# Performance work log

Measured on AMD Instinct MI355X. Metric: run time of the kernel, lower is better.

Reference implementation:

```python
import jax, jax.numpy as jnp
import numpy as np

N, E, IN, HID, OUT = 50000, 800000, 128, 256, 128
NMASK = 25000  # int(0.5 * N)
EPS = 1e-5


def setup_inputs() -> dict:
    key = jax.random.key(0)
    ks = jax.random.split(key, 8)

    def glorot(k, shape):
        lim = float(np.sqrt(6.0 / (shape[0] + shape[1])))
        return jax.random.uniform(k, shape, jnp.float32, -lim, lim)

    x = jax.random.normal(ks[0], (N, IN), jnp.float32)
    edge_index = jax.random.randint(ks[1], (2, E), 0, N, dtype=jnp.int32)
    mask_nodes = jax.random.permutation(ks[2], N)[:NMASK].astype(jnp.int32)
    return {
        "x": x,
        "edge_index": edge_index,
        "mask_nodes": mask_nodes,
        "mask_token": jnp.zeros((IN,), jnp.float32),
        "W1": glorot(ks[3], (IN, HID)), "b1": jnp.zeros((HID,), jnp.float32),
        "g1": jnp.ones((HID,), jnp.float32), "be1": jnp.zeros((HID,), jnp.float32),
        "a1": jnp.full((1,), 0.25, jnp.float32),
        "W2": glorot(ks[4], (HID, OUT)), "b2": jnp.zeros((OUT,), jnp.float32),
        "g2": jnp.ones((OUT,), jnp.float32), "be2": jnp.zeros((OUT,), jnp.float32),
        "a2": jnp.full((1,), 0.25, jnp.float32),
        "Wd": glorot(ks[5], (OUT, IN)), "bd": jnp.zeros((IN,), jnp.float32),
        "gd": jnp.ones((IN,), jnp.float32), "bed": jnp.zeros((IN,), jnp.float32),
        "ad": jnp.full((1,), 0.25, jnp.float32),
    }


def _gcn_conv(h, W, b, src, dst, dinv):
    # PyG GCNConv with self-loops: out = D^-1/2 (A+I) D^-1/2 (h W) + b
    h = h @ W
    coef = dinv[src] * dinv[dst]                      # [E]
    agg = jnp.zeros_like(h).at[dst].add(h[src] * coef[:, None])
    agg = agg + h * (dinv * dinv)[:, None]            # self-loop term
    return agg + b


def _bn_prelu(h, g, be, a):
    # BatchNorm (training-mode batch stats, biased var) + PReLU
    mu = jnp.mean(h, axis=0)
    var = jnp.mean((h - mu) ** 2, axis=0)
    h = (h - mu) * jax.lax.rsqrt(var + EPS) * g + be
    return jnp.where(h >= 0, h, a * h)


def reference(x, edge_index, mask_nodes, mask_token,
              W1, b1, g1, be1, a1,
              W2, b2, g2, be2, a2,
              Wd, bd, gd, bed, ad):
    src, dst = edge_index[0], edge_index[1]
    # degree with self-loops (shared by all conv layers on the same graph)
    deg = jnp.zeros((N,), x.dtype).at[dst].add(1.0) + 1.0
    dinv = jax.lax.rsqrt(deg)

    target = jax.lax.stop_gradient(x[mask_nodes])      # detached recon target

    # mask: x[mask] = 0 then += token  ->  set to token
    h = x.at[mask_nodes].set(mask_token)

    # online encoder: 2 layers of GCNConv -> BN -> PReLU
    h = _bn_prelu(_gcn_conv(h, W1, b1, src, dst, dinv), g1, be1, a1)
    h = _bn_prelu(_gcn_conv(h, W2, b2, src, dst, dinv), g2, be2, a2)

    # re-mask encoded representation
    h = h.at[mask_nodes].set(0.0)

    # decoder: 1 layer
    re_x = _bn_prelu(_gcn_conv(h, Wd, bd, src, dst, dinv), gd, bed, ad)

    # sce loss (alpha=1) on masked nodes
    p = re_x[mask_nodes]
    p = p / jnp.maximum(jnp.linalg.norm(p, axis=-1, keepdims=True), 1e-12)
    t = target / jnp.maximum(jnp.linalg.norm(target, axis=-1, keepdims=True), 1e-12)
    loss = jnp.mean(1.0 - jnp.sum(p * t, axis=-1))
    return loss
```

## Files before the change

### kernel.cpp

```cpp
#include <hip/hip_runtime.h>
#include <hip/hip_bf16.h>
#include <math.h>


#define EPSV 1e-5f
#define CAP2 16
#define DCAP 64

typedef __attribute__((ext_vector_type(8))) short short8v;
typedef __attribute__((ext_vector_type(4))) float f32x4;
typedef __attribute__((ext_vector_type(2))) float f32x2;

static __device__ __forceinline__ void atomAddF(float* p, float v) {
  unsafeAtomicAdd(p, v);
}

static __device__ __forceinline__ unsigned short f2bf(float f) {
  union { float f; unsigned u; } v; v.f = f;
  unsigned u = v.u;
  u += 0x7fffu + ((u >> 16) & 1u);
  return (unsigned short)(u >> 16);
}
static __device__ __forceinline__ float bflo(unsigned w) {
  union { unsigned u; float f; } v; v.u = w << 16; return v.f;
}
static __device__ __forceinline__ float bfhi(unsigned w) {
  union { unsigned u; float f; } v; v.u = w & 0xffff0000u; return v.f;
}
static __device__ __forceinline__ unsigned char f2fp8(float f) {
  int p = __builtin_amdgcn_cvt_pk_fp8_f32(f, 0.0f, 0, false);
  return (unsigned char)(p & 0xff);
}

__global__ void fill_f32(float* __restrict__ p, float v, int n) {
  int i = blockIdx.x * blockDim.x + threadIdx.x;
  if (i < n) p[i] = v;
}

__global__ void init_ws(int* __restrict__ cursor, int* __restrict__ maskflag,
                        float* __restrict__ sums, int N) {
  int i = blockIdx.x * blockDim.x + threadIdx.x;
  if (i < 8 * N) cursor[i] = 0;
  if (i < N) maskflag[i] = 0;
  if (i < 512) sums[i] = 0.0f;
}

#define EPB2 512
__global__ __launch_bounds__(256) void fill_slots_priv(const int* __restrict__ src,
                                                       const int* __restrict__ dst,
                                                       int* __restrict__ cursor,
                                                       unsigned short* __restrict__ slots,
                                                       int E, int N) {
  int p = blockIdx.x & 7;
  int* __restrict__ cur = cursor + (size_t)p * N;
  unsigned short* __restrict__ sl = slots + (size_t)p * N * CAP2;
  int base = blockIdx.x * EPB2 + threadIdx.x * 2;
  if (base + 1 < E) {
    int2 d = *reinterpret_cast<const int2*>(dst + base);
    int2 s = *reinterpret_cast<const int2*>(src + base);
    int pos0 = atomicAdd(&cur[d.x], 1);
    int pos1 = atomicAdd(&cur[d.y], 1);
    if (pos0 < CAP2) sl[d.x * CAP2 + pos0] = (unsigned short)s.x;
    if (pos1 < CAP2) sl[d.y * CAP2 + pos1] = (unsigned short)s.y;
  } else if (base < E) {
    int d = dst[base];
    int pos = atomicAdd(&cur[d], 1);
    if (pos < CAP2) sl[d * CAP2 + pos] = (unsigned short)src[base];
  }
}

__global__ void finalize_graph(const int* __restrict__ cursor, float* __restrict__ dinv,
                               uint2* __restrict__ cnts8, int N) {
  int i = blockIdx.x * blockDim.x + threadIdx.x;
  if (i >= N) return;
  int tot = 0;
  unsigned lo = 0, hi = 0;
  #pragma unroll
  for (int p = 0; p < 8; ++p) {
    int cv = cursor[(size_t)p * N + i];
    tot += cv;
    unsigned cl = (unsigned)min(cv, CAP2);
    if (p < 4) lo |= cl << (p * 8);
    else       hi |= cl << ((p - 4) * 8);
  }
  dinv[i] = rsqrtf((float)tot + 1.0f);
  cnts8[i] = make_uint2(lo, hi);
}

__global__ void cast_mask8(const float* __restrict__ x, const float* __restrict__ token,
                           const int* __restrict__ maskflag,
                           unsigned char* __restrict__ b, int n8) {
  int i = blockIdx.x * blockDim.x + threadIdx.x;
  if (i >= n8) return;
  int node = (i * 8) >> 7;
  int col = (i * 8) & 127;
  const float* srcp = maskflag[node] ? (token + col) : (x + i * 8);
  float4 v0 = *reinterpret_cast<const float4*>(srcp);
  float4 v1 = *reinterpret_cast<const float4*>(srcp + 4);
  int lo = 0, hi = 0;
  lo = __builtin_amdgcn_cvt_pk_fp8_f32(v0.x, v0.y, lo, false);
  lo = __builtin_amdgcn_cvt_pk_fp8_f32(v0.z, v0.w, lo, true);
  hi = __builtin_amdgcn_cvt_pk_fp8_f32(v1.x, v1.y, hi, false);
  hi = __builtin_amdgcn_cvt_pk_fp8_f32(v1.z, v1.w, hi, true);
  *reinterpret_cast<uint2*>(b + (size_t)i * 8) = make_uint2((unsigned)lo, (unsigned)hi);
}

__global__ void set_flags(const int* __restrict__ mask, int* __restrict__ flag, int nmask) {
  int i = blockIdx.x * blockDim.x + threadIdx.x;
  if (i < nmask) flag[mask[i]] = 1;
}

__global__ void pack_all(const float* __restrict__ W1, const float* __restrict__ W2,
                         const float* __restrict__ Wd, unsigned short* __restrict__ W1p,
                         unsigned short* __restrict__ W2p, unsigned short* __restrict__ Wdp) {
  int idx = blockIdx.x * blockDim.x + threadIdx.x;
  const float* w; unsigned short* o; int Nn; int rel;
  if (idx < 32768)      { w = W1; o = W1p; Nn = 256; rel = idx; }
  else if (idx < 65536) { w = W2; o = W2p; Nn = 128; rel = idx - 32768; }
  else if (idx < 81920) { w = Wd; o = Wdp; Nn = 128; rel = idx - 65536; }
  else return;
  int k = rel / Nn, n = rel % Nn;
  o[((size_t)(k >> 3) * Nn + n) * 8 + (k & 7)] = f2bf(w[rel]);
}

__global__ __launch_bounds__(256) void gather_fp8(const unsigned char* __restrict__ hw8,
                                                  const uint2* __restrict__ cnts8,
                                                  const unsigned short* __restrict__ slots,
                                                  const float* __restrict__ dinv,
                                                  unsigned short* __restrict__ out, int N) {
  __shared__ int ds[16][DCAP];
  int g = threadIdx.x >> 4, lane = threadIdx.x & 15;
  int node = blockIdx.x * 16 + g;
  if (node >= N) node = N - 1;
  float di = dinv[node];
  uint2 cc = cnts8[node];
  int c[8] = { (int)(cc.x & 255), (int)((cc.x >> 8) & 255),
               (int)((cc.x >> 16) & 255), (int)(cc.x >> 24),
               (int)(cc.y & 255), (int)((cc.y >> 8) & 255),
               (int)((cc.y >> 16) & 255), (int)(cc.y >> 24) };
  int tot = c[0] + c[1] + c[2] + c[3] + c[4] + c[5] + c[6] + c[7];
  if (tot > DCAP) tot = DCAP;
  if (lane < 8) {
    int p = lane;
    int pre = 0;
    #pragma unroll
    for (int q = 0; q < 8; ++q) pre += (q < p) ? c[q] : 0;
    const unsigned short* sp = slots + ((size_t)p * N + node) * CAP2;
    int cp = c[p];
    for (int j = 0; j < cp; ++j) {
      int idx = pre + j;
      if (idx < DCAP) ds[g][idx] = (int)sp[j];
    }
  }
  __syncthreads();

  float c0 = di * di;
  float acc[8];
  {
    uint2 v = *reinterpret_cast<const uint2*>(hw8 + (size_t)node * 128 + lane * 8);
    f32x2 a0 = __builtin_amdgcn_cvt_pk_f32_fp8(v.x, false);
    f32x2 a1 = __builtin_amdgcn_cvt_pk_f32_fp8(v.x, true);
    f32x2 a2 = __builtin_amdgcn_cvt_pk_f32_fp8(v.y, false);
    f32x2 a3 = __builtin_amdgcn_cvt_pk_f32_fp8(v.y, true);
    acc[0] = c0 * a0[0]; acc[1] = c0 * a0[1];
    acc[2] = c0 * a1[0]; acc[3] = c0 * a1[1];
    acc[4] = c0 * a2[0]; acc[5] = c0 * a2[1];
    acc[6] = c0 * a3[0]; acc[7] = c0 * a3[1];
  }
  int j = 0;
  for (; j + 8 <= tot; j += 8) {
    int sv[8];
    #pragma unroll
    for (int t = 0; t < 8; ++t) sv[t] = ds[g][j + t];
    float cf[8]; uint2 u[8];
    #pragma unroll
    for (int t = 0; t < 8; ++t) {
      cf[t] = dinv[sv[t]] * di;
      u[t] = *reinterpret_cast<const uint2*>(hw8 + (size_t)sv[t] * 128 + lane * 8);
    }
    #pragma unroll
    for (int t = 0; t < 8; ++t) {
      f32x2 a0 = __builtin_amdgcn_cvt_pk_f32_fp8(u[t].x, false);
      f32x2 a1 = __builtin_amdgcn_cvt_pk_f32_fp8(u[t].x, true);
      f32x2 a2 = __builtin_amdgcn_cvt_pk_f32_fp8(u[t].y, false);
      f32x2 a3 = __builtin_amdgcn_cvt_pk_f32_fp8(u[t].y, true);
      acc[0] += cf[t] * a0[0]; acc[1] += cf[t] * a0[1];
      acc[2] += cf[t] * a1[0]; acc[3] += cf[t] * a1[1];
      acc[4] += cf[t] * a2[0]; acc[5] += cf[t] * a2[1];
      acc[6] += cf[t] * a3[0]; acc[7] += cf[t] * a3[1];
    }
  }
  for (; j < tot; ++j) {
    int s0 = ds[g][j];
    float ca = dinv[s0] * di;
    uint2 u0 = *reinterpret_cast<const uint2*>(hw8 + (size_t)s0 * 128 + lane * 8);
    f32x2 a0 = __builtin_amdgcn_cvt_pk_f32_fp8(u0.x, false);
    f32x2 a1 = __builtin_amdgcn_cvt_pk_f32_fp8(u0.x, true);
    f32x2 a2 = __builtin_amdgcn_cvt_pk_f32_fp8(u0.y, false);
    f32x2 a3 = __builtin_amdgcn_cvt_pk_f32_fp8(u0.y, true);
    acc[0] += ca * a0[0]; acc[1] += ca * a0[1];
    acc[2] += ca * a1[0]; acc[3] += ca * a1[1];
    acc[4] += ca * a2[0]; acc[5] += ca * a2[1];
    acc[6] += ca * a3[0]; acc[7] += ca * a3[1];
  }
  uint4 o;
  o.x = ((unsigned)f2bf(acc[1]) << 16) | f2bf(acc[0]);
  o.y = ((unsigned)f2bf(acc[3]) << 16) | f2bf(acc[2]);
  o.z = ((unsigned)f2bf(acc[5]) << 16) | f2bf(acc[4]);
  o.w = ((unsigned)f2bf(acc[7]) << 16) | f2bf(acc[6]);
  *reinterpret_cast<uint4*>(out + (size_t)node * 128 + lane * 8) = o;
}

template <int MODE, int OUT8>
__global__ __launch_bounds__(256) void gemm_bf16(const unsigned short* __restrict__ A,
                                                 const unsigned short* __restrict__ Bp,
                                                 void* __restrict__ Cout,
                                                 const float* __restrict__ scale,
                                                 const float* __restrict__ shift,
                                                 const float* __restrict__ alpha,
                                                 const int* __restrict__ maskflag,
                                                 int M, int K, int Nn) {
  __shared__ unsigned short As[64][32];
  __shared__ unsigned short Bs[4][64][8];
  int tid = threadIdx.x;
  int m0 = blockIdx.y * 64;
  int n0 = blockIdx.x * 64;
  int lane = tid & 63, w = tid >> 6;
  int wr = w >> 1, wc = w & 1;
  int colq = lane & 15, chq = lane >> 4;

  float aval = 0.25f;
  if constexpr (MODE > 0) aval = alpha[0];

  f32x4 acc[2][2] = {};

  int arow = tid >> 2, ach = tid & 3;
  int grow = m0 + arow;
  int bch = tid >> 6, bn = tid & 63;

  for (int k0 = 0; k0 < K; k0 += 32) {
    {
      uint4 raw = make_uint4(0, 0, 0, 0);
      bool valid = (grow < M);
      if constexpr (MODE == 2) {
        if (valid && maskflag[grow]) valid = false;
      }
      if (valid)
        raw = *reinterpret_cast<const uint4*>(A + (size_t)grow * K + k0 + ach * 8);
      if constexpr (MODE > 0) {
        int kk = k0 + ach * 8;
        float4 sc0 = *reinterpret_cast<const float4*>(scale + kk);
        float4 sc1 = *reinterpret_cast<const float4*>(scale + kk + 4);
        float4 sh0 = *reinterpret_cast<const float4*>(shift + kk);
        float4 sh1 = *reinterpret_cast<const float4*>(shift + kk + 4);
        float f0 = bflo(raw.x) * sc0.x + sh0.x;
        float f1 = bfhi(raw.x) * sc0.y + sh0.y;
        float f2 = bflo(raw.y) * sc0.z + sh0.z;
        float f3 = bfhi(raw.y) * sc0.w + sh0.w;
        float f4 = bflo(raw.z) * sc1.x + sh1.x;
        float f5 = bfhi(raw.z) * sc1.y + sh1.y;
        float f6 = bflo(raw.w) * sc1.z + sh1.z;
        float f7 = bfhi(raw.w) * sc1.w + sh1.w;
        f0 = f0 >= 0.f ? f0 : aval * f0;  f1 = f1 >= 0.f ? f1 : aval * f1;
        f2 = f2 >= 0.f ? f2 : aval * f2;  f3 = f3 >= 0.f ? f3 : aval * f3;
        f4 = f4 >= 0.f ? f4 : aval * f4;  f5 = f5 >= 0.f ? f5 : aval * f5;
        f6 = f6 >= 0.f ? f6 : aval * f6;  f7 = f7 >= 0.f ? f7 : aval * f7;
        if (!valid) { f0=f1=f2=f3=f4=f5=f6=f7=0.f; }
        raw.x = ((unsigned)f2bf(f1) << 16) | f2bf(f0);
        raw.y = ((unsigned)f2bf(f3) << 16) | f2bf(f2);
        raw.z = ((unsigned)f2bf(f5) << 16) | f2bf(f4);
        raw.w = ((unsigned)f2bf(f7) << 16) | f2bf(f6);
      }
      *reinterpret_cast<uint4*>(&As[arow][ach * 8]) = raw;
    }
    {
      uint4 bv = *reinterpret_cast<const uint4*>(
          Bp + (((size_t)(k0 >> 3) + bch) * Nn + n0 + bn) * 8);
      *reinterpret_cast<uint4*>(&Bs[bch][bn][0]) = bv;
    }
    __syncthreads();

    short8v afrag[2], bfrag[2];
    #pragma unroll
    for (int mi = 0; mi < 2; ++mi)
      afrag[mi] = *reinterpret_cast<const short8v*>(&As[wr * 32 + mi * 16 + colq][chq * 8]);
    #pragma unroll
    for (int ni = 0; ni < 2; ++ni)
      bfrag[ni] = *reinterpret_cast<const short8v*>(&Bs[chq][wc * 32 + ni * 16 + colq][0]);
    #pragma unroll
    for (int mi = 0; mi < 2; ++mi)
      #pragma unroll
      for (int ni = 0; ni < 2; ++ni)
        acc[mi][ni] = __builtin_amdgcn_mfma_f32_16x16x32_bf16(afrag[mi], bfrag[ni],
                                                              acc[mi][ni], 0, 0, 0);
    __syncthreads();
  }

  int rbase = (lane >> 4) * 4;
  #pragma unroll
  for (int mi = 0; mi < 2; ++mi) {
    #pragma unroll
    for (int i = 0; i < 4; ++i) {
      int row = m0 + wr * 32 + mi * 16 + rbase + i;
      if (row < M) {
        #pragma unroll
        for (int ni = 0; ni < 2; ++ni) {
          size_t idx = (size_t)row * Nn + n0 + wc * 32 + ni * 16 + colq;
          if constexpr (OUT8) {
            ((unsigned char*)Cout)[idx] = f2fp8(acc[mi][ni][i]);
          } else {
            ((unsigned short*)Cout)[idx] = f2bf(acc[mi][ni][i]);
          }
        }
      }
    }
  }
}

__global__ __launch_bounds__(256) void bn_stats_bf(const unsigned short* __restrict__ h,
                                                   float* __restrict__ sums,
                                                   int Nrows, int F) {
  __shared__ float sm[4096];
  int FC = F >> 3;
  int RG = 256 / FC;
  int fc = threadIdx.x % FC;
  int rg = threadIdx.x / FC;
  float s[8] = {}, s2[8] = {};
  for (int r = blockIdx.x * RG + rg; r < Nrows; r += gridDim.x * RG) {
    uint4 v = *reinterpret_cast<const uint4*>(h + (size_t)r * F + fc * 8);
    float f[8] = { bflo(v.x), bfhi(v.x), bflo(v.y), bfhi(v.y),
                   bflo(v.z), bfhi(v.z), bflo(v.w), bfhi(v.w) };
    #pragma unroll
    for (int j = 0; j < 8; ++j) { s[j] += f[j]; s2[j] += f[j] * f[j]; }
  }
  #pragma unroll
  for (int j = 0; j < 8; ++j) {
    sm[rg * F + fc * 8 + j] = s[j];
    sm[2048 + rg * F + fc * 8 + j] = s2[j];
  }
  __syncthreads();
  if (threadIdx.x < F) {
    float t = 0.f, t2 = 0.f;
    for (int g = 0; g < RG; ++g) {
      t += sm[g * F + threadIdx.x];
      t2 += sm[2048 + g * F + threadIdx.x];
    }
    atomAddF(&sums[threadIdx.x], t);
    atomAddF(&sums[F + threadIdx.x], t2);
  }
}

__global__ void bn_finalize(float* __restrict__ sums, const float* __restrict__ g,
                            const float* __restrict__ be, float* __restrict__ scale,
                            float* __restrict__ shift, int Nrows, int F) {
  int f = blockIdx.x * blockDim.x + threadIdx.x;
  if (f < F) {
    float inv_n = 1.0f / (float)Nrows;
    float mu = sums[f] * inv_n;
    float var = sums[F + f] * inv_n - mu * mu;
    float sc = g[f] * rsqrtf(var + EPSV);
    scale[f] = sc;
    shift[f] = be[f] - mu * sc;
    sums[f] = 0.0f;
    sums[F + f] = 0.0f;
  }
}

__global__ __launch_bounds__(256) void loss_fused(const unsigned short* __restrict__ agg,
                                                  const float* __restrict__ x,
                                                  const int* __restrict__ mask,
                                                  const float* __restrict__ scale,
                                                  const float* __restrict__ shift,
                                                  const float* __restrict__ alpha,
                                                  float* __restrict__ out, int nmask) {
  int lane = threadIdx.x & 63;
  int wid = threadIdx.x >> 6;
  int gw = blockIdx.x * 4 + wid;
  int nw = gridDim.x * 4;
  float a = alpha[0];
  float2 sc = *reinterpret_cast<const float2*>(scale + lane * 2);
  float2 sh = *reinterpret_cast<const float2*>(shift + lane * 2);
  float local = 0.f;
  for (int i = gw; i < nmask; i += nw) {
    int node = mask[i];
    unsigned pw = *reinterpret_cast<const unsigned*>(agg + (size_t)node * 128 + lane * 2);
    float2 tv = *reinterpret_cast<const float2*>(x + (size_t)node * 128 + lane * 2);
    float p0 = bflo(pw) * sc.x + sh.x; p0 = p0 >= 0.f ? p0 : a * p0;
    float p1 = bfhi(pw) * sc.y + sh.y; p1 = p1 >= 0.f ? p1 : a * p1;
    float pp = p0 * p0 + p1 * p1;
    float tt = tv.x * tv.x + tv.y * tv.y;
    float pt = p0 * tv.x + p1 * tv.y;
    #pragma unroll
    for (int o = 32; o > 0; o >>= 1) {
      pp += __shfl_xor(pp, o);
      tt += __shfl_xor(tt, o);
      pt += __shfl_xor(pt, o);
    }
    if (lane == 0)
      local += 1.0f - pt / (fmaxf(sqrtf(pp), 1e-12f) * fmaxf(sqrtf(tt), 1e-12f));
  }
  __shared__ float wsum[4];
  if (lane == 0) wsum[wid] = local;
  __syncthreads();
  if (threadIdx.x == 0) {
    float s = wsum[0] + wsum[1] + wsum[2] + wsum[3];
    atomAddF(out, s / (float)nmask);
  }
}

static inline int cdiv(int a, int b) { return (a + b - 1) / b; }

extern "C" void kernel_launch(void* const* d_in, const int* in_sizes, int n_in,
                              void* d_out, int out_size, void* d_ws, size_t ws_size,
                              hipStream_t stream) {
  const float* x     = (const float*)d_in[0];
  const int*   ei    = (const int*)d_in[1];
  const int*   mask  = (const int*)d_in[2];
  const float* token = (const float*)d_in[3];
  const float* W1 = (const float*)d_in[4];
  const float* g1 = (const float*)d_in[6];
  const float* be1 = (const float*)d_in[7];
  const float* a1 = (const float*)d_in[8];
  const float* W2 = (const float*)d_in[9];
  const float* g2 = (const float*)d_in[11];
  const float* be2 = (const float*)d_in[12];
  const float* a2 = (const float*)d_in[13];
  const float* Wd = (const float*)d_in[14];
  const float* gd = (const float*)d_in[16];
  const float* bed = (const float*)d_in[17];
  const float* ad = (const float*)d_in[18];
  float* out = (float*)d_out;

  const int IN = 128, HID = 256;
  const int N = in_sizes[0] / IN;
  const int E = in_sizes[1] / 2;
  const int NMASK = in_sizes[2];
  const int* src = ei;
  const int* dst = ei + E;

  char* wp = (char*)d_ws;
  size_t off = 0;
  auto alloc = [&](size_t bytes) -> char* {
    char* p = wp + off;
    off = (off + bytes + 255) & ~(size_t)255;
    return p;
  };
  unsigned short* B1 = (unsigned short*)alloc((size_t)N * 128 * 2);
  unsigned short* B2 = (unsigned short*)alloc((size_t)N * 128 * 2);
  unsigned short* B4 = (unsigned short*)alloc((size_t)N * 128 * 2);
  unsigned short* B3 = (unsigned short*)alloc((size_t)N * 256 * 2);
  unsigned char* F8A = (unsigned char*)alloc((size_t)N * 128);
  unsigned char* F8B = (unsigned char*)alloc((size_t)N * 128);
  float* dinv  = (float*)alloc((size_t)N * 4);
  float* sums  = (float*)alloc(512 * 4);
  float* sc1   = (float*)alloc(256 * 4);
  float* sh1   = (float*)alloc(256 * 4);
  float* sc2   = (float*)alloc(256 * 4);
  float* sh2   = (float*)alloc(256 * 4);
  float* scd   = (float*)alloc(256 * 4);
  float* shd   = (float*)alloc(256 * 4);
  int* cursor   = (int*)alloc((size_t)8 * N * 4);
  unsigned short* slots = (unsigned short*)alloc((size_t)8 * N * CAP2 * 2);
  uint2* cnts8  = (uint2*)alloc((size_t)N * 8);
  int* maskflag = (int*)alloc((size_t)N * 4);
  unsigned short* W1p = (unsigned short*)alloc((size_t)IN * HID * 2);
  unsigned short* W2p = (unsigned short*)alloc((size_t)HID * IN * 2);
  unsigned short* Wdp = (unsigned short*)alloc((size_t)IN * IN * 2);

  init_ws<<<cdiv(8 * N, 256), 256, 0, stream>>>(cursor, maskflag, sums, N);
  fill_slots_priv<<<cdiv(E, EPB2), 256, 0, stream>>>(src, dst, cursor, slots, E, N);
  finalize_graph<<<cdiv(N, 256), 256, 0, stream>>>(cursor, dinv, cnts8, N);
  set_flags<<<cdiv(NMASK, 256), 256, 0, stream>>>(mask, maskflag, NMASK);
  pack_all<<<cdiv(IN * HID + HID * IN + IN * IN, 256), 256, 0, stream>>>(
      W1, W2, Wd, W1p, W2p, Wdp);

  cast_mask8<<<cdiv(N * IN / 8, 256), 256, 0, stream>>>(x, token, maskflag, F8B, N * IN / 8);

  gather_fp8<<<cdiv(N, 16), 256, 0, stream>>>(F8B, cnts8, slots, dinv, B2, N);
  gemm_bf16<0, 0><<<dim3(HID / 64, cdiv(N, 64)), 256, 0, stream>>>(
      B2, W1p, B3, nullptr, nullptr, nullptr, nullptr, N, IN, HID);
  bn_stats_bf<<<128, 256, 0, stream>>>(B3, sums, N, HID);
  bn_finalize<<<1, 256, 0, stream>>>(sums, g1, be1, sc1, sh1, N, HID);

  gemm_bf16<1, 1><<<dim3(IN / 64, cdiv(N, 64)), 256, 0, stream>>>(
      B3, W2p, F8A, sc1, sh1, a1, nullptr, N, HID, IN);
  gather_fp8<<<cdiv(N, 16), 256, 0, stream>>>(F8A, cnts8, slots, dinv, B1, N);
  bn_stats_bf<<<128, 256, 0, stream>>>(B1, sums, N, IN);
  bn_finalize<<<1, 256, 0, stream>>>(sums, g2, be2, sc2, sh2, N, IN);

  gemm_bf16<2, 1><<<dim3(IN / 64, cdiv(N, 64)), 256, 0, stream>>>(
      B1, Wdp, F8A, sc2, sh2, a2, maskflag, N, IN, IN);
  gather_fp8<<<cdiv(N, 16), 256, 0, stream>>>(F8A, cnts8, slots, dinv, B4, N);
  bn_stats_bf<<<128, 256, 0, stream>>>(B4, sums, N, IN);
  bn_finalize<<<1, 256, 0, stream>>>(sums, gd, bed, scd, shd, N, IN);

  fill_f32<<<1, 64, 0, stream>>>(out, 0.0f, 1);
  loss_fused<<<256, 256, 0, stream>>>(B4, x, mask, scd, shd, ad, out, NMASK);
}
```

Baseline: 338.8 us.

## Fuse BatchNorm statistics into GEMM and gather epilogues, store layer-1 output as fp8

Removes the separate bn_stats passes. BatchNorm column sums and sums of squares are now computed in the epilogues of the first GEMM and the gather kernels, written as per-block partials to a scratch buffer, and folded by a small reduce_stats kernel. The layer-1 GEMM output is stored as fp8 instead of bf16, and the next GEMM reads fp8 directly, which halves that intermediate's traffic. In exchange it adds shared-memory reductions and an extra sync in the epilogues, and the fp8 intermediate loses precision. Stats are taken from fp32 accumulators before rounding, which differs slightly from the old reads of rounded bf16 values.

```diff
diff --git a/kernel.cpp b/kernel.cpp
--- a/kernel.cpp
+++ b/kernel.cpp
@@ -123,15 +123,30 @@
   o[((size_t)(k >> 3) * Nn + n) * 8 + (k & 7)] = f2bf(w[rel]);
 }
 
+__global__ void reduce_stats(const float* __restrict__ scratch, float* __restrict__ sums,
+                             int P, int G, int W, int F) {
+  int c = threadIdx.x;
+  if (c >= W) return;
+  int g0 = blockIdx.x % G, s0 = blockIdx.x / G;
+  int f = g0 * (W >> 1) + (c >> 1);
+  float s = 0.f;
+  for (int r = g0 + G * s0; r < P; r += G * 32)
+    s += scratch[(size_t)r * W + c];
+  atomAddF(&sums[(c & 1) ? F + f : f], s);
+}
+
+template <int STATS>
 __global__ __launch_bounds__(256) void gather_fp8(const unsigned char* __restrict__ hw8,
                                                   const uint2* __restrict__ cnts8,
                                                   const unsigned short* __restrict__ slots,
                                                   const float* __restrict__ dinv,
-                                                  unsigned short* __restrict__ out, int N) {
+                                                  unsigned short* __restrict__ out,
+                                                  float* __restrict__ scratch, int N) {
   __shared__ int ds[16][DCAP];
+  __shared__ float val[128][17];
   int g = threadIdx.x >> 4, lane = threadIdx.x & 15;
-  int node = blockIdx.x * 16 + g;
-  if (node >= N) node = N - 1;
+  int node0 = blockIdx.x * 16 + g;
+  int node = (node0 < N) ? node0 : (N - 1);
   float di = dinv[node];
   uint2 cc = cnts8[node];
   int c[8] = { (int)(cc.x & 255), (int)((cc.x >> 8) & 255),
@@ -203,25 +218,46 @@
     acc[4] += ca * a2[0]; acc[5] += ca * a2[1];
     acc[6] += ca * a3[0]; acc[7] += ca * a3[1];
   }
-  uint4 o;
-  o.x = ((unsigned)f2bf(acc[1]) << 16) | f2bf(acc[0]);
-  o.y = ((unsigned)f2bf(acc[3]) << 16) | f2bf(acc[2]);
-  o.z = ((unsigned)f2bf(acc[5]) << 16) | f2bf(acc[4]);
-  o.w = ((unsigned)f2bf(acc[7]) << 16) | f2bf(acc[6]);
-  *reinterpret_cast<uint4*>(out + (size_t)node * 128 + lane * 8) = o;
-}
-
-template <int MODE, int OUT8>
-__global__ __launch_bounds__(256) void gemm_bf16(const unsigned short* __restrict__ A,
+  if (node0 < N) {
+    uint4 o;
+    o.x = ((unsigned)f2bf(acc[1]) << 16) | f2bf(acc[0]);
+    o.y = ((unsigned)f2bf(acc[3]) << 16) | f2bf(acc[2]);
+    o.z = ((unsigned)f2bf(acc[5]) << 16) | f2bf(acc[4]);
+    o.w = ((unsigned)f2bf(acc[7]) << 16) | f2bf(acc[6]);
+    *reinterpret_cast<uint4*>(out + (size_t)node * 128 + lane * 8) = o;
+  }
+  if constexpr (STATS) {
+    bool nv = (node0 < N);
+    #pragma unroll
+    for (int jj = 0; jj < 8; ++jj)
+      val[lane * 8 + jj][g] = nv ? acc[jj] : 0.f;
+    __syncthreads();
+    if (threadIdx.x < 128) {
+      float S = 0.f, S2 = 0.f;
+      #pragma unroll
+      for (int q = 0; q < 16; ++q) {
+        float v = val[threadIdx.x][q];
+        S += v; S2 += v * v;
+      }
+      scratch[(size_t)blockIdx.x * 256 + threadIdx.x * 2] = S;
+      scratch[(size_t)blockIdx.x * 256 + threadIdx.x * 2 + 1] = S2;
+    }
+  }
+}
+
+template <int MODE, int OUT8, int A8, int STATS>
+__global__ __launch_bounds__(256) void gemm_bf16(const void* __restrict__ A_,
                                                  const unsigned short* __restrict__ Bp,
                                                  void* __restrict__ Cout,
                                                  const float* __restrict__ scale,
                                                  const float* __restrict__ shift,
                                                  const float* __restrict__ alpha,
                                                  const int* __restrict__ maskflag,
+                                                 float* __restrict__ scratch,
                                                  int M, int K, int Nn) {
   __shared__ unsigned short As[64][32];
   __shared__ unsigned short Bs[4][64][8];
+  __shared__ float sred[64][8][2];
   int tid = threadIdx.x;
   int m0 = blockIdx.y * 64;
   int n0 = blockIdx.x * 64;
@@ -245,22 +281,40 @@
       if constexpr (MODE == 2) {
         if (valid && maskflag[grow]) valid = false;
       }
-      if (valid)
-        raw = *reinterpret_cast<const uint4*>(A + (size_t)grow * K + k0 + ach * 8);
-      if constexpr (MODE > 0) {
+      if constexpr (MODE == 0) {
+        if (valid)
+          raw = *reinterpret_cast<const uint4*>(
+              (const unsigned short*)A_ + (size_t)grow * K + k0 + ach * 8);
+      } else {
+        float f0, f1, f2, f3, f4, f5, f6, f7;
+        if constexpr (A8) {
+          uint2 r8 = make_uint2(0, 0);
+          if (valid)
+            r8 = *reinterpret_cast<const uint2*>(
+                (const unsigned char*)A_ + (size_t)grow * K + k0 + ach * 8);
+          f32x2 p0 = __builtin_amdgcn_cvt_pk_f32_fp8(r8.x, false);
+          f32x2 p1 = __builtin_amdgcn_cvt_pk_f32_fp8(r8.x, true);
+          f32x2 p2 = __builtin_amdgcn_cvt_pk_f32_fp8(r8.y, false);
+          f32x2 p3 = __builtin_amdgcn_cvt_pk_f32_fp8(r8.y, true);
+          f0 = p0[0]; f1 = p0[1]; f2 = p1[0]; f3 = p1[1];
+          f4 = p2[0]; f5 = p2[1]; f6 = p3[0]; f7 = p3[1];
+        } else {
+          uint4 t = make_uint4(0, 0, 0, 0);
+          if (valid)
+            t = *reinterpret_cast<const uint4*>(
+                (const unsigned short*)A_ + (size_t)grow * K + k0 + ach * 8);
+          f0 = bflo(t.x); f1 = bfhi(t.x); f2 = bflo(t.y); f3 = bfhi(t.y);
+          f4 = bflo(t.z); f5 = bfhi(t.z); f6 = bflo(t.w); f7 = bfhi(t.w);
+        }
         int kk = k0 + ach * 8;
         float4 sc0 = *reinterpret_cast<const float4*>(scale + kk);
         float4 sc1 = *reinterpret_cast<const float4*>(scale + kk + 4);
         float4 sh0 = *reinterpret_cast<const float4*>(shift + kk);
         float4 sh1 = *reinterpret_cast<const float4*>(shift + kk + 4);
-        float f0 = bflo(raw.x) * sc0.x + sh0.x;
-        float f1 = bfhi(raw.x) * sc0.y + sh0.y;
-        float f2 = bflo(raw.y) * sc0.z + sh0.z;
-        float f3 = bfhi(raw.y) * sc0.w + sh0.w;
-        float f4 = bflo(raw.z) * sc1.x + sh1.x;
-        float f5 = bfhi(raw.z) * sc1.y + sh1.y;
-        float f6 = bflo(raw.w) * sc1.z + sh1.z;
-        float f7 = bfhi(raw.w) * sc1.w + sh1.w;
+        f0 = f0 * sc0.x + sh0.x; f1 = f1 * sc0.y + sh0.y;
+        f2 = f2 * sc0.z + sh0.z; f3 = f3 * sc0.w + sh0.w;
+        f4 = f4 * sc1.x + sh1.x; f5 = f5 * sc1.y + sh1.y;
+        f6 = f6 * sc1.z + sh1.z; f7 = f7 * sc1.w + sh1.w;
         f0 = f0 >= 0.f ? f0 : aval * f0;  f1 = f1 >= 0.f ? f1 : aval * f1;
         f2 = f2 >= 0.f ? f2 : aval * f2;  f3 = f3 >= 0.f ? f3 : aval * f3;
         f4 = f4 >= 0.f ? f4 : aval * f4;  f5 = f5 >= 0.f ? f5 : aval * f5;
@@ -315,38 +369,31 @@
       }
     }
   }
-}
-
-__global__ __launch_bounds__(256) void bn_stats_bf(const unsigned short* __restrict__ h,
-                                                   float* __restrict__ sums,
-                                                   int Nrows, int F) {
-  __shared__ float sm[4096];
-  int FC = F >> 3;
-  int RG = 256 / FC;
-  int fc = threadIdx.x % FC;
-  int rg = threadIdx.x / FC;
-  float s[8] = {}, s2[8] = {};
-  for (int r = blockIdx.x * RG + rg; r < Nrows; r += gridDim.x * RG) {
-    uint4 v = *reinterpret_cast<const uint4*>(h + (size_t)r * F + fc * 8);
-    float f[8] = { bflo(v.x), bfhi(v.x), bflo(v.y), bfhi(v.y),
-                   bflo(v.z), bfhi(v.z), bflo(v.w), bfhi(v.w) };
-    #pragma unroll
-    for (int j = 0; j < 8; ++j) { s[j] += f[j]; s2[j] += f[j] * f[j]; }
-  }
-  #pragma unroll
-  for (int j = 0; j < 8; ++j) {
-    sm[rg * F + fc * 8 + j] = s[j];
-    sm[2048 + rg * F + fc * 8 + j] = s2[j];
-  }
-  __syncthreads();
-  if (threadIdx.x < F) {
-    float t = 0.f, t2 = 0.f;
-    for (int g = 0; g < RG; ++g) {
-      t += sm[g * F + threadIdx.x];
-      t2 += sm[2048 + g * F + threadIdx.x];
-    }
-    atomAddF(&sums[threadIdx.x], t);
-    atomAddF(&sums[F + threadIdx.x], t2);
+
+  if constexpr (STATS) {
+    #pragma unroll
+    for (int ni = 0; ni < 2; ++ni) {
+      int col_l = wc * 32 + ni * 16 + colq;
+      float s = 0.f, s2 = 0.f;
+      #pragma unroll
+      for (int mi = 0; mi < 2; ++mi)
+        #pragma unroll
+        for (int i = 0; i < 4; ++i) {
+          float v = acc[mi][ni][i];
+          s += v; s2 += v * v;
+        }
+      sred[col_l][wr * 4 + (lane >> 4)][0] = s;
+      sred[col_l][wr * 4 + (lane >> 4)][1] = s2;
+    }
+    __syncthreads();
+    if (tid < 64) {
+      float S = 0.f, S2 = 0.f;
+      #pragma unroll
+      for (int k = 0; k < 8; ++k) { S += sred[tid][k][0]; S2 += sred[tid][k][1]; }
+      size_t r = (size_t)blockIdx.y * gridDim.x + blockIdx.x;
+      scratch[r * 128 + tid * 2] = S;
+      scratch[r * 128 + tid * 2 + 1] = S2;
+    }
   }
 }
 
@@ -437,6 +484,8 @@
   const int NMASK = in_sizes[2];
   const int* src = ei;
   const int* dst = ei + E;
+  const int MB = cdiv(N, 64);
+  const int GB = cdiv(N, 16);
 
   char* wp = (char*)d_ws;
   size_t off = 0;
@@ -448,9 +497,11 @@
   unsigned short* B1 = (unsigned short*)alloc((size_t)N * 128 * 2);
   unsigned short* B2 = (unsigned short*)alloc((size_t)N * 128 * 2);
   unsigned short* B4 = (unsigned short*)alloc((size_t)N * 128 * 2);
-  unsigned short* B3 = (unsigned short*)alloc((size_t)N * 256 * 2);
+  unsigned char* F8C = (unsigned char*)alloc((size_t)N * 256);
   unsigned char* F8A = (unsigned char*)alloc((size_t)N * 128);
   unsigned char* F8B = (unsigned char*)alloc((size_t)N * 128);
+  float* scrG = (float*)alloc((size_t)(4 * MB) * 128 * 4);
+  float* scrA = (float*)alloc((size_t)GB * 256 * 4);
   float* dinv  = (float*)alloc((size_t)N * 4);
   float* sums  = (float*)alloc(512 * 4);
   float* sc1   = (float*)alloc(256 * 4);
@@ -476,22 +527,22 @@
 
   cast_mask8<<<cdiv(N * IN / 8, 256), 256, 0, stream>>>(x, token, maskflag, F8B, N * IN / 8);
 
-  gather_fp8<<<cdiv(N, 16), 256, 0, stream>>>(F8B, cnts8, slots, dinv, B2, N);
-  gemm_bf16<0, 0><<<dim3(HID / 64, cdiv(N, 64)), 256, 0, stream>>>(
-      B2, W1p, B3, nullptr, nullptr, nullptr, nullptr, N, IN, HID);
-  bn_stats_bf<<<128, 256, 0, stream>>>(B3, sums, N, HID);
+  gather_fp8<0><<<GB, 256, 0, stream>>>(F8B, cnts8, slots, dinv, B2, nullptr, N);
+  gemm_bf16<0, 1, 0, 1><<<dim3(HID / 64, MB), 256, 0, stream>>>(
+      B2, W1p, F8C, nullptr, nullptr, nullptr, nullptr, scrG, N, IN, HID);
+  reduce_stats<<<4 * 32, 128, 0, stream>>>(scrG, sums, 4 * MB, 4, 128, HID);
   bn_finalize<<<1, 256, 0, stream>>>(sums, g1, be1, sc1, sh1, N, HID);
 
-  gemm_bf16<1, 1><<<dim3(IN / 64, cdiv(N, 64)), 256, 0, stream>>>(
-      B3, W2p, F8A, sc1, sh1, a1, nullptr, N, HID, IN);
-  gather_fp8<<<cdiv(N, 16), 256, 0, stream>>>(F8A, cnts8, slots, dinv, B1, N);
-  bn_stats_bf<<<128, 256, 0, stream>>>(B1, sums, N, IN);
+  gemm_bf16<1, 1, 1, 0><<<dim3(IN / 64, MB), 256, 0, stream>>>(
+      F8C, W2p, F8A, sc1, sh1, a1, nullptr, nullptr, N, HID, IN);
+  gather_fp8<1><<<GB, 256, 0, stream>>>(F8A, cnts8, slots, dinv, B1, scrA, N);
+  reduce_stats<<<32, 256, 0, stream>>>(scrA, sums, GB, 1, 256, IN);
   bn_finalize<<<1, 256, 0, stream>>>(sums, g2, be2, sc2, sh2, N, IN);
 
-  gemm_bf16<2, 1><<<dim3(IN / 64, cdiv(N, 64)), 256, 0, stream>>>(
-      B1, Wdp, F8A, sc2, sh2, a2, maskflag, N, IN, IN);
-  gather_fp8<<<cdiv(N, 16), 256, 0, stream>>>(F8A, cnts8, slots, dinv, B4, N);
-  bn_stats_bf<<<128, 256, 0, stream>>>(B4, sums, N, IN);
+  gemm_bf16<2, 1, 0, 0><<<dim3(IN / 64, MB), 256, 0, stream>>>(
+      B1, Wdp, F8B, sc2, sh2, a2, maskflag, nullptr, N, IN, IN);
+  gather_fp8<1><<<GB, 256, 0, stream>>>(F8B, cnts8, slots, dinv, B4, scrA, N);
+  reduce_stats<<<32, 256, 0, stream>>>(scrA, sums, GB, 1, 256, IN);
   bn_finalize<<<1, 256, 0, stream>>>(sums, gd, bed, scd, shd, N, IN);
 
   fill_f32<<<1, 64, 0, stream>>>(out, 0.0f, 1);
```

Measured after the change: 356.2 us. 5.1% more time.
